# Optimization experiments

Hardware: AMD Instinct MI355X
Metric: run time of the kernel (lower is better)

Reference implementation:

```python
import jax, jax.numpy as jnp
import numpy as np

B, T, E, H, M2 = 8, 2048, 256, 2, 134
HD = E // H


def setup_inputs() -> dict:
    key = jax.random.key(0)
    ks = jax.random.split(key, 10)
    s = 0.02
    return {
        "X": jax.random.normal(ks[0], (B, T, E), dtype=jnp.float32),
        "Y": jax.random.uniform(ks[1], (B, M2), dtype=jnp.float32),
        "wpe": s * jax.random.normal(ks[2], (T, E), dtype=jnp.float32),
        "ln1_g": jnp.ones((E,), jnp.float32), "ln1_b": jnp.zeros((E,), jnp.float32),
        "attn_w": s * jax.random.normal(ks[3], (3 * E, E), dtype=jnp.float32),
        "attn_b": jnp.zeros((3 * E,), jnp.float32),
        "attnproj_w": s * jax.random.normal(ks[4], (E, E), dtype=jnp.float32),
        "attnproj_b": jnp.zeros((E,), jnp.float32),
        "ln2_g": jnp.ones((E,), jnp.float32), "ln2_b": jnp.zeros((E,), jnp.float32),
        "fc_w": s * jax.random.normal(ks[5], (2 * E, E), dtype=jnp.float32),
        "fc_b": jnp.zeros((2 * E,), jnp.float32),
        "mlpproj_w": s * jax.random.normal(ks[6], (E, 2 * E), dtype=jnp.float32),
        "mlpproj_b": jnp.zeros((E,), jnp.float32),
        "lnf_g": jnp.ones((E,), jnp.float32), "lnf_b": jnp.zeros((E,), jnp.float32),
        "head_w": s * jax.random.normal(ks[7], (M2, E), dtype=jnp.float32),
        "head_b": jnp.zeros((M2,), jnp.float32),
    }


def _ln(x, g, b, eps=1e-5):
    mu = x.mean(-1, keepdims=True)
    var = ((x - mu) ** 2).mean(-1, keepdims=True)
    return (x - mu) * jax.lax.rsqrt(var + eps) * g + b


def reference(X, Y, wpe, ln1_g, ln1_b, attn_w, attn_b, attnproj_w, attnproj_b,
              ln2_g, ln2_b, fc_w, fc_b, mlpproj_w, mlpproj_b, lnf_g, lnf_b,
              head_w, head_b):
    # positional ids = arange(T) -> wpe itself; cls ids = [0]*T/2 + [1]*T/2
    cls_ids = np.concatenate([np.zeros(T // 2, np.int32), np.ones(T // 2, np.int32)])
    x = X + wpe + wpe[cls_ids]                      # [B,T,E] (dropout = identity, eval)

    # single Block (n_layer=1), preceded by ReLU as in cross_mod loop
    x = jax.nn.relu(x)
    h = _ln(x, ln1_g, ln1_b)
    qkv = h @ attn_w.T + attn_b                     # [B,T,3E]
    q, k, v = jnp.split(qkv, 3, axis=-1)
    q, k, v = jax.nn.relu(q), jax.nn.relu(k), jax.nn.relu(v)
    split_heads = lambda t: t.reshape(B, T, H, HD).transpose(0, 2, 1, 3)
    q, k, v = split_heads(q), split_heads(k), split_heads(v)
    att = jnp.einsum('bhqd,bhkd->bhqk', q, k) * (1.0 / np.sqrt(HD))
    tril = jnp.tril(jnp.ones((T, T), dtype=bool))
    # masked_fill(-inf) then ReLU  ==  zero outside causal mask, ReLU inside
    att = jnp.where(tril, jax.nn.relu(att), 0.0)    # [B,H,T,T]
    y = jnp.einsum('bhqk,bhkd->bhqd', att, v)
    y = y.transpose(0, 2, 1, 3).reshape(B, T, E)
    x = x + (y @ attnproj_w.T + attnproj_b)

    h = _ln(x, ln2_g, ln2_b)
    x = x + (jax.nn.relu(h @ fc_w.T + fc_b) @ mlpproj_w.T + mlpproj_b)

    x = jax.nn.relu(x)
    x = _ln(x, lnf_g, lnf_b)
    x = jax.nn.relu(x)
    emb = x.mean(axis=1)                            # [B,E]
    logits = jax.nn.relu(emb @ head_w.T + head_b)   # [B,M2]

    loss1 = jnp.sqrt(jnp.mean((logits - Y) ** 2))
    e1, e2 = emb[:, : E // 2], emb[:, E // 2:]
    loss3 = jnp.sqrt(jnp.mean((e1 - e2) ** 2))
    loss = 50.0 * loss1 + loss3
    return (e1, e2, loss, loss1, loss3, logits)
```

## Files before the change

### kernel.cpp

```cpp
#include <hip/hip_runtime.h>
#include <hip/hip_bf16.h>

#define Bc 8
#define Tc 2048
#define Ec 256
#define Hc 2
#define HDc 128
#define Mrows (Bc*Tc)
#define M2c 134

using bfx8  = __attribute__((ext_vector_type(8))) __bf16;
using f32x4 = __attribute__((ext_vector_type(4))) float;

__device__ __forceinline__ void gll16(const __bf16* g, __bf16* lds) {
    __builtin_amdgcn_global_load_lds(
        (const __attribute__((address_space(1))) unsigned int*)g,
        (__attribute__((address_space(3))) unsigned int*)lds, 16, 0, 0);
}

__global__ __launch_bounds__(256) void embed_prep_k(const float* X, const float* wpe,
                                                    const float* g, const float* bb,
                                                    const float* attn_w, const float* apw,
                                                    const float* fcw, const float* mpw,
                                                    __bf16* wb, float* embsum,
                                                    __bf16* xres, __bf16* hb) {
    int m = blockIdx.x;
    int e = threadIdx.x;
    if (m < 2048) {
        int i = m * 256 + e;
        if (i < 196608)       wb[i] = (__bf16)attn_w[i];
        else if (i < 262144)  wb[i] = (__bf16)apw[i - 196608];
        else if (i < 393216)  wb[i] = (__bf16)fcw[i - 262144];
        else                  wb[i] = (__bf16)mpw[i - 393216];
        if (m < 8) embsum[m * 256 + e] = 0.f;
    }
    int t = m & (Tc - 1);
    float v = X[(size_t)m * Ec + e] + wpe[(size_t)t * Ec + e] + wpe[(size_t)(t >= 1024) * Ec + e];
    v = fmaxf(v, 0.f);
    xres[(size_t)m * Ec + e] = (__bf16)v;
    float s1 = v, s2 = v * v;
    #pragma unroll
    for (int o = 32; o; o >>= 1) { s1 += __shfl_xor(s1, o, 64); s2 += __shfl_xor(s2, o, 64); }
    __shared__ float a1[4], a2[4];
    int w = threadIdx.x >> 6;
    if ((threadIdx.x & 63) == 0) { a1[w] = s1; a2[w] = s2; }
    __syncthreads();
    float m1 = (a1[0] + a1[1] + a1[2] + a1[3]) * (1.f / 256.f);
    float m2 = (a2[0] + a2[1] + a2[2] + a2[3]) * (1.f / 256.f);
    float r = rsqrtf(m2 - m1 * m1 + 1e-5f);
    hb[(size_t)m * Ec + e] = (__bf16)((v - m1) * r * g[e] + bb[e]);
}

__global__ __launch_bounds__(256) void gemm_qkv(const __bf16* __restrict__ A,
                                                const __bf16* __restrict__ Bw,
                                                const float* __restrict__ bias,
                                                __bf16* __restrict__ Qb,
                                                __bf16* __restrict__ Kb,
                                                __bf16* __restrict__ Vb) {
    const int K = 256;
    __shared__ __bf16 As[128 * 64];
    __shared__ __bf16 Bs[128 * 64];
    const int tid = threadIdx.x, w = tid >> 6, l = tid & 63;
    const int m0 = blockIdx.y * 128, n0 = blockIdx.x * 128;
    const int wr = w >> 1, wc = w & 1;
    const int quad = l >> 4, col15 = l & 15;

    f32x4 acc[4][4];
    f32x4 zz = {0.f, 0.f, 0.f, 0.f};
    #pragma unroll
    for (int i = 0; i < 4; i++)
        #pragma unroll
        for (int j = 0; j < 4; j++) acc[i][j] = zz;

    const int lrow = l >> 3;
    const int pbs  = l & 7;

    for (int kb = 0; kb < K; kb += 64) {
        #pragma unroll
        for (int it = 0; it < 4; it++) {
            int chunk = w * 4 + it;
            int row = chunk * 8 + lrow;
            int lb = pbs ^ (row & 7);
            gll16(A  + (size_t)(m0 + row) * K + kb + lb * 8, As + chunk * 512);
            gll16(Bw + (size_t)(n0 + row) * K + kb + lb * 8, Bs + chunk * 512);
        }
        __syncthreads();
        #pragma unroll
        for (int ks = 0; ks < 2; ks++) {
            bfx8 af[4], bfr[4];
            #pragma unroll
            for (int rt = 0; rt < 4; rt++) {
                int row = wr * 64 + rt * 16 + col15;
                int pb = (ks * 4 + quad) ^ (row & 7);
                af[rt] = *(const bfx8*)(As + row * 64 + pb * 8);
            }
            #pragma unroll
            for (int ct = 0; ct < 4; ct++) {
                int row = wc * 64 + ct * 16 + col15;
                int pb = (ks * 4 + quad) ^ (row & 7);
                bfr[ct] = *(const bfx8*)(Bs + row * 64 + pb * 8);
            }
            #pragma unroll
            for (int rt = 0; rt < 4; rt++)
                #pragma unroll
                for (int ct = 0; ct < 4; ct++)
                    acc[rt][ct] = __builtin_amdgcn_mfma_f32_16x16x32_bf16(af[rt], bfr[ct], acc[rt][ct], 0, 0, 0);
        }
        __syncthreads();
    }

    #pragma unroll
    for (int rt = 0; rt < 4; rt++)
        #pragma unroll
        for (int ct = 0; ct < 4; ct++) {
            int mgb = m0 + wr * 64 + rt * 16 + quad * 4;
            int ng  = n0 + wc * 64 + ct * 16 + col15;
            float bsv = bias[ng];
            #pragma unroll
            for (int r = 0; r < 4; r++) {
                float val = fmaxf(acc[rt][ct][r] + bsv, 0.f);
                int mg = mgb + r;
                int sel = ng >> 8;
                int hh = (ng >> 7) & 1;
                int d = ng & 127;
                int bb = mg >> 11, tt = mg & (Tc - 1);
                size_t idx = ((size_t)((bb * 2 + hh) * Tc + tt)) * HDc + d;
                __bf16 bv = (__bf16)val;
                if (sel == 0) Qb[idx] = bv;
                else if (sel == 1) Kb[idx] = bv;
                else Vb[idx] = bv;
            }
        }
}

__global__ __launch_bounds__(256) void transpose_v(const unsigned short* Vb, unsigned short* Vt) {
    __shared__ unsigned short tile[64][66];
    int kt = blockIdx.x, dt = blockIdx.y, bh = blockIdx.z;
    int tid = threadIdx.x;
    int k0 = kt * 64, d0 = dt * 64;
    int rr = tid >> 4, cc = (tid & 15) * 4;
    #pragma unroll
    for (int p = 0; p < 4; p++) {
        int k = p * 16 + rr;
        const unsigned short* src = Vb + ((size_t)(bh * Tc + k0 + k)) * HDc + d0 + cc;
        ushort4 vv = *(const ushort4*)src;
        tile[k][cc] = vv.x; tile[k][cc + 1] = vv.y; tile[k][cc + 2] = vv.z; tile[k][cc + 3] = vv.w;
    }
    __syncthreads();
    #pragma unroll
    for (int p = 0; p < 4; p++) {
        int d = p * 16 + rr;
        unsigned short* dst = Vt + ((size_t)(bh * HDc + d0 + d)) * Tc + k0 + cc;
        ushort4 ov;
        ov.x = tile[cc][d]; ov.y = tile[cc + 1][d]; ov.z = tile[cc + 2][d]; ov.w = tile[cc + 3][d];
        *(ushort4*)dst = ov;
    }
}

__global__ __launch_bounds__(512, 4) void attn6_k(const __bf16* __restrict__ Qb,
                                                  const __bf16* __restrict__ Kb,
                                                  const __bf16* __restrict__ Vt,
                                                  __bf16* __restrict__ Y1,
                                                  __bf16* __restrict__ Y2,
                                                  __bf16* __restrict__ Y3,
                                                  __bf16* __restrict__ Y4) {
    __shared__ __bf16 Ks[2][64 * 128];
    __shared__ __bf16 Vs[2][64 * 128];
    __shared__ __bf16 Ss[128 * 64];
    int bid = blockIdx.x;
    int lane8 = bid & 7;
    int s = bid >> 3;
    int bh = ((s & 1) << 3) | lane8;
    int f = s >> 1;
    int qt, ch;
    if (f < 16)      { qt = 12 + (f >> 2);          ch = f & 3; }
    else if (f < 28) { int r = f - 16; int d3 = r / 3; qt = 8 + d3; ch = r - 3 * d3; }
    else if (f < 36) { qt = 4 + ((f - 28) >> 1);    ch = (f - 28) & 1; }
    else             { qt = f - 36;                 ch = 0; }
    int Q0 = qt * 128;
    int kts = ch * 8;
    int kte = min(kts + 8, 2 * qt + 2);

    int tid = threadIdx.x, w = tid >> 6, l = tid & 63;
    int quad = l >> 4, col15 = l & 15;
    const int qs = w >> 1, kh = w & 1;
    const int lrowK = l >> 4, pbsK = l & 15;
    const int lrowV = l >> 3, pbsV = l & 7;

    __bf16* Qs = &Ks[0][0];
    #pragma unroll
    for (int it = 0; it < 4; it++) {
        int chunk = w * 4 + it;
        int row = chunk * 4 + lrowK;
        int lb = pbsK ^ (row & 7);
        gll16(Qb + ((size_t)(bh * Tc + Q0 + row)) * HDc + lb * 8, Qs + chunk * 512);
    }
    __syncthreads();
    bfx8 qf[2][4];
    #pragma unroll
    for (int rt = 0; rt < 2; rt++)
        #pragma unroll
        for (int ks = 0; ks < 4; ks++) {
            int row = qs * 32 + rt * 16 + col15;
            int pb = (ks * 4 + quad) ^ (row & 7);
            qf[rt][ks] = *(const bfx8*)(Qs + row * 128 + pb * 8);
        }
    __syncthreads();

    f32x4 zz = {0.f, 0.f, 0.f, 0.f};
    f32x4 yacc[2][4];
    #pragma unroll
    for (int rt = 0; rt < 2; rt++)
        #pragma unroll
        for (int dt = 0; dt < 4; dt++) yacc[rt][dt] = zz;

    auto stageKV = [&](int buf, int kt) {
        #pragma unroll
        for (int it = 0; it < 2; it++) {
            int chunk = w * 2 + it;
            int rowK = chunk * 4 + lrowK;
            int lbK = pbsK ^ (rowK & 7);
            gll16(Kb + ((size_t)(bh * Tc + kt * 64 + rowK)) * HDc + lbK * 8, Ks[buf] + chunk * 512);
            int rowV = chunk * 8 + lrowV;
            int lbV = pbsV ^ (rowV & 7);
            gll16(Vt + ((size_t)(bh * HDc + rowV)) * Tc + kt * 64 + lbV * 8, Vs[buf] + chunk * 512);
        }
    };

    stageKV(0, kts);
    int cur = 0;
    for (int kt = kts; kt < kte; kt++) {
        __syncthreads();
        if (kt + 1 < kte) stageKV(cur ^ 1, kt + 1);

        f32x4 sacc[2][2];
        #pragma unroll
        for (int rt = 0; rt < 2; rt++)
            #pragma unroll
            for (int ct = 0; ct < 2; ct++) sacc[rt][ct] = zz;
        #pragma unroll
        for (int ks = 0; ks < 4; ks++) {
            #pragma unroll
            for (int ct = 0; ct < 2; ct++) {
                int row = kh * 32 + ct * 16 + col15;
                int pb = (ks * 4 + quad) ^ (row & 7);
                bfx8 kf = *(const bfx8*)(Ks[cur] + row * 128 + pb * 8);
                #pragma unroll
                for (int rt = 0; rt < 2; rt++)
                    sacc[rt][ct] = __builtin_amdgcn_mfma_f32_16x16x32_bf16(qf[rt][ks], kf, sacc[rt][ct], 0, 0, 0);
            }
        }

        #pragma unroll
        for (int ct = 0; ct < 2; ct++) {
            int kl = kh * 32 + ct * 16 + col15;
            int kg = kt * 64 + kl;
            int blk = kl >> 3, off = kl & 7;
            #pragma unroll
            for (int rt = 0; rt < 2; rt++)
                #pragma unroll
                for (int r = 0; r < 4; r++) {
                    int qlw = qs * 32 + rt * 16 + quad * 4 + r;
                    float val = (kg <= Q0 + qlw) ? fmaxf(sacc[rt][ct][r], 0.f) : 0.f;
                    int pb = blk ^ (qlw & 7);
                    Ss[qlw * 64 + pb * 8 + off] = (__bf16)val;
                }
        }

        asm volatile("s_waitcnt lgkmcnt(0)" ::: "memory");
        __builtin_amdgcn_s_barrier();
        __builtin_amdgcn_sched_barrier(0);

        #pragma unroll
        for (int ks = 0; ks < 2; ks++) {
            bfx8 sf[2];
            #pragma unroll
            for (int rt = 0; rt < 2; rt++) {
                int rowS = qs * 32 + rt * 16 + col15;
                int pbS = (ks * 4 + quad) ^ (rowS & 7);
                sf[rt] = *(const bfx8*)(Ss + rowS * 64 + pbS * 8);
            }
            #pragma unroll
            for (int dt = 0; dt < 4; dt++) {
                int rowV = kh * 64 + dt * 16 + col15;
                int pb = (ks * 4 + quad) ^ (rowV & 7);
                bfx8 vf = *(const bfx8*)(Vs[cur] + rowV * 64 + pb * 8);
                #pragma unroll
                for (int rt = 0; rt < 2; rt++)
                    yacc[rt][dt] = __builtin_amdgcn_mfma_f32_16x16x32_bf16(sf[rt], vf, yacc[rt][dt], 0, 0, 0);
            }
        }
        cur ^= 1;
    }

    __bf16* Yp = (ch == 0) ? Y1 : (ch == 1) ? Y2 : (ch == 2) ? Y3 : Y4;
    int b = bh >> 1, h = bh & 1;
    const float sc = 0.08838834764831845f;
    #pragma unroll
    for (int rt = 0; rt < 2; rt++)
        #pragma unroll
        for (int dt = 0; dt < 4; dt++) {
            int d = kh * 64 + dt * 16 + col15;
            #pragma unroll
            for (int r = 0; r < 4; r++) {
                int q = Q0 + qs * 32 + rt * 16 + quad * 4 + r;
                Yp[((size_t)(b * Tc + q)) * Ec + h * HDc + d] = (__bf16)(yacc[rt][dt][r] * sc);
            }
        }
}

__global__ __launch_bounds__(512, 1) void mega_k(const __bf16* __restrict__ Y1,
                                                 const __bf16* __restrict__ Y2,
                                                 const __bf16* __restrict__ Y3,
                                                 const __bf16* __restrict__ Y4,
                                                 const __bf16* __restrict__ wap,
                                                 const float* __restrict__ apb,
                                                 const __bf16* __restrict__ xres,
                                                 const float* __restrict__ ln2_g,
                                                 const float* __restrict__ ln2_b,
                                                 const __bf16* __restrict__ wfc,
                                                 const float* __restrict__ fcb,
                                                 const __bf16* __restrict__ wmp,
                                                 const float* __restrict__ mpb,
                                                 const float* __restrict__ lnf_g,
                                                 const float* __restrict__ lnf_b,
                                                 float* __restrict__ embsum) {
    __shared__ __bf16 h2s[4 * 4096];
    __shared__ __bf16 fc64[8 * 4096];
    __shared__ __bf16 Bs[256 * 64];
    __shared__ float ps1[64][8], ps2[64][8];
    __shared__ float mus[64], rss[64];
    const int tid = threadIdx.x, w = tid >> 6, l = tid & 63;
    const int m0 = blockIdx.x * 64;
    const int quad = l >> 4, col15 = l & 15;
    const int lrow = l >> 3, pbs = l & 7;
    const int n0 = w * 32;
    f32x4 zz = {0.f, 0.f, 0.f, 0.f};

    const int nsum = (((m0 & (Tc - 1)) >> 6) + 8) >> 3;
    __bf16* As = fc64;

    const int arow_s = tid >> 3;
    const int ablk   = tid & 7;

    auto loadY = [&](int kb) -> bfx8 {
        size_t off = (size_t)(m0 + arow_s) * 256 + kb + ablk * 8;
        bfx8 a1 = *(const bfx8*)(Y1 + off);
        float tmp[8];
        #pragma unroll
        for (int jj = 0; jj < 8; jj++) tmp[jj] = (float)a1[jj];
        if (nsum > 1) { bfx8 aj = *(const bfx8*)(Y2 + off);
            #pragma unroll
            for (int jj = 0; jj < 8; jj++) tmp[jj] += (float)aj[jj]; }
        if (nsum > 2) { bfx8 aj = *(const bfx8*)(Y3 + off);
            #pragma unroll
            for (int jj = 0; jj < 8; jj++) tmp[jj] += (float)aj[jj]; }
        if (nsum > 3) { bfx8 aj = *(const bfx8*)(Y4 + off);
            #pragma unroll
            for (int jj = 0; jj < 8; jj++) tmp[jj] += (float)aj[jj]; }
        #pragma unroll
        for (int jj = 0; jj < 8; jj++) a1[jj] = (__bf16)tmp[jj];
        return a1;
    };

    f32x4 acc[4][2];
    #pragma unroll
    for (int rt = 0; rt < 4; rt++)
        #pragma unroll
        for (int ct = 0; ct < 2; ct++) acc[rt][ct] = zz;

    bfx8 av = loadY(0);

    for (int kb = 0; kb < 256; kb += 64) {
        __syncthreads();
        { int pb = ablk ^ (arow_s & 7);
          *(bfx8*)(As + arow_s * 64 + pb * 8) = av; }
        #pragma unroll
        for (int it = 0; it < 4; it++) {
            int chunk = w * 4 + it;
            int row = chunk * 8 + lrow;
            int lb = pbs ^ (row & 7);
            gll16(wap + (size_t)row * 256 + kb + lb * 8, Bs + chunk * 512);
        }
        bfx8 avn;
        if (kb < 192) avn = loadY(kb + 64);
        __syncthreads();
        #pragma unroll
        for (int ks = 0; ks < 2; ks++) {
            bfx8 af[4];
            #pragma unroll
            for (int rt = 0; rt < 4; rt++) {
                int ar = rt * 16 + col15;
                int apbk = (ks * 4 + quad) ^ (ar & 7);
                af[rt] = *(const bfx8*)(As + ar * 64 + apbk * 8);
            }
            #pragma unroll
            for (int ct = 0; ct < 2; ct++) {
                int br = n0 + ct * 16 + col15;
                int bpb = (ks * 4 + quad) ^ (br & 7);
                bfx8 bf = *(const bfx8*)(Bs + br * 64 + bpb * 8);
                #pragma unroll
                for (int rt = 0; rt < 4; rt++)
                    acc[rt][ct] = __builtin_amdgcn_mfma_f32_16x16x32_bf16(af[rt], bf, acc[rt][ct], 0, 0, 0);
            }
        }
        if (kb < 192) av = avn;
    }

    float xv[4][2][4];
    #pragma unroll
    for (int ct = 0; ct < 2; ct++) {
        int ng = n0 + ct * 16 + col15;
        float bsv = apb[ng];
        #pragma unroll
        for (int rt = 0; rt < 4; rt++)
            #pragma unroll
            for (int r = 0; r < 4; r++) {
                int mg = m0 + rt * 16 + quad * 4 + r;
                xv[rt][ct][r] = acc[rt][ct][r] + bsv + (float)xres[(size_t)mg * 256 + ng];
            }
    }
    #pragma unroll
    for (int rt = 0; rt < 4; rt++)
        #pragma unroll
        for (int r = 0; r < 4; r++) {
            float a  = xv[rt][0][r] + xv[rt][1][r];
            float b2 = xv[rt][0][r] * xv[rt][0][r] + xv[rt][1][r] * xv[rt][1][r];
            #pragma unroll
            for (int o = 1; o < 16; o <<= 1) { a += __shfl_xor(a, o, 64); b2 += __shfl_xor(b2, o, 64); }
            if (col15 == 0) { int row = rt * 16 + quad * 4 + r; ps1[row][w] = a; ps2[row][w] = b2; }
        }
    __syncthreads();
    {
        int row = tid >> 3, widx = tid & 7;
        float a = ps1[row][widx], b2 = ps2[row][widx];
        #pragma unroll
        for (int o = 1; o < 8; o <<= 1) { a += __shfl_xor(a, o, 64); b2 += __shfl_xor(b2, o, 64); }
        if ((l & 7) == 0) {
            float mu = a * (1.f / 256.f);
            float var = b2 * (1.f / 256.f) - mu * mu;
            mus[row] = mu; rss[row] = rsqrtf(var + 1e-5f);
        }
    }
    __syncthreads();
    #pragma unroll
    for (int ct = 0; ct < 2; ct++) {
        int ng = n0 + ct * 16 + col15;
        float gv = ln2_g[ng], bv = ln2_b[ng];
        int panel = ng >> 6, c = ng & 63;
        #pragma unroll
        for (int rt = 0; rt < 4; rt++)
            #pragma unroll
            for (int r = 0; r < 4; r++) {
                int row = rt * 16 + quad * 4 + r;
                float h = (xv[rt][ct][r] - mus[row]) * rss[row] * gv + bv;
                h2s[panel * 4096 + row * 64 + ((c >> 3) ^ (row & 7)) * 8 + (c & 7)] = (__bf16)h;
            }
    }

    for (int half = 0; half < 2; half++) {
        f32x4 acc2[4][2];
        #pragma unroll
        for (int rt = 0; rt < 4; rt++)
            #pragma unroll
            for (int ct = 0; ct < 2; ct++) acc2[rt][ct] = zz;
        for (int kb = 0; kb < 256; kb += 64) {
            __syncthreads();
            #pragma unroll
            for (int it = 0; it < 4; it++) {
                int chunk = w * 4 + it;
                int row = chunk * 8 + lrow;
                int lb = pbs ^ (row & 7);
                gll16(wfc + (size_t)(half * 256 + row) * 256 + kb + lb * 8, Bs + chunk * 512);
            }
            __syncthreads();
            int panel = kb >> 6;
            #pragma unroll
            for (int ks = 0; ks < 2; ks++) {
                bfx8 af[4];
                #pragma unroll
                for (int rt = 0; rt < 4; rt++) {
                    int ar = rt * 16 + col15;
                    int apbk = (ks * 4 + quad) ^ (ar & 7);
                    af[rt] = *(const bfx8*)(h2s + panel * 4096 + ar * 64 + apbk * 8);
                }
                #pragma unroll
                for (int ct = 0; ct < 2; ct++) {
                    int br = n0 + ct * 16 + col15;
                    int bpb = (ks * 4 + quad) ^ (br & 7);
                    bfx8 bf = *(const bfx8*)(Bs + br * 64 + bpb * 8);
                    #pragma unroll
                    for (int rt = 0; rt < 4; rt++)
                        acc2[rt][ct] = __builtin_amdgcn_mfma_f32_16x16x32_bf16(af[rt], bf, acc2[rt][ct], 0, 0, 0);
                }
            }
        }
        #pragma unroll
        for (int ct = 0; ct < 2; ct++) {
            int col = half * 256 + n0 + ct * 16 + col15;
            float bsv = fcb[col];
            int panel = col >> 6, c = col & 63;
            #pragma unroll
            for (int rt = 0; rt < 4; rt++)
                #pragma unroll
                for (int r = 0; r < 4; r++) {
                    int row = rt * 16 + quad * 4 + r;
                    float val = fmaxf(acc2[rt][ct][r] + bsv, 0.f);
                    fc64[panel * 4096 + row * 64 + ((c >> 3) ^ (row & 7)) * 8 + (c & 7)] = (__bf16)val;
                }
        }
    }

    #pragma unroll
    for (int rt = 0; rt < 4; rt++)
        #pragma unroll
        for (int ct = 0; ct < 2; ct++) acc[rt][ct] = zz;
    for (int kb = 0; kb < 512; kb += 64) {
        __syncthreads();
        #pragma unroll
        for (int it = 0; it < 4; it++) {
            int chunk = w * 4 + it;
            int row = chunk * 8 + lrow;
            int lb = pbs ^ (row & 7);
            gll16(wmp + (size_t)row * 512 + kb + lb * 8, Bs + chunk * 512);
        }
        __syncthreads();
        int panel = kb >> 6;
        #pragma unroll
        for (int ks = 0; ks < 2; ks++) {
            bfx8 af[4];
            #pragma unroll
            for (int rt = 0; rt < 4; rt++) {
                int ar = rt * 16 + col15;
                int apbk = (ks * 4 + quad) ^ (ar & 7);
                af[rt] = *(const bfx8*)(fc64 + panel * 4096 + ar * 64 + apbk * 8);
            }
            #pragma unroll
            for (int ct = 0; ct < 2; ct++) {
                int br = n0 + ct * 16 + col15;
                int bpb = (ks * 4 + quad) ^ (br & 7);
                bfx8 bf = *(const bfx8*)(Bs + br * 64 + bpb * 8);
                #pragma unroll
                for (int rt = 0; rt < 4; rt++)
                    acc[rt][ct] = __builtin_amdgcn_mfma_f32_16x16x32_bf16(af[rt], bf, acc[rt][ct], 0, 0, 0);
            }
        }
    }

    #pragma unroll
    for (int ct = 0; ct < 2; ct++) {
        int ng = n0 + ct * 16 + col15;
        float bsv = mpb[ng];
        #pragma unroll
        for (int rt = 0; rt < 4; rt++)
            #pragma unroll
            for (int r = 0; r < 4; r++)
                xv[rt][ct][r] = fmaxf(acc[rt][ct][r] + bsv + xv[rt][ct][r], 0.f);
    }
    #pragma unroll
    for (int rt = 0; rt < 4; rt++)
        #pragma unroll
        for (int r = 0; r < 4; r++) {
            float a  = xv[rt][0][r] + xv[rt][1][r];
            float b2 = xv[rt][0][r] * xv[rt][0][r] + xv[rt][1][r] * xv[rt][1][r];
            #pragma unroll
            for (int o = 1; o < 16; o <<= 1) { a += __shfl_xor(a, o, 64); b2 += __shfl_xor(b2, o, 64); }
            if (col15 == 0) { int row = rt * 16 + quad * 4 + r; ps1[row][w] = a; ps2[row][w] = b2; }
        }
    __syncthreads();
    {
        int row = tid >> 3, widx = tid & 7;
        float a = ps1[row][widx], b2 = ps2[row][widx];
        #pragma unroll
        for (int o = 1; o < 8; o <<= 1) { a += __shfl_xor(a, o, 64); b2 += __shfl_xor(b2, o, 64); }
        if ((l & 7) == 0) {
            float mu = a * (1.f / 256.f);
            float var = b2 * (1.f / 256.f) - mu * mu;
            mus[row] = mu; rss[row] = rsqrtf(var + 1e-5f);
        }
    }
    __syncthreads();
    #pragma unroll
    for (int ct = 0; ct < 2; ct++) {
        int ng = n0 + ct * 16 + col15;
        float gv = lnf_g[ng], bv = lnf_b[ng];
        float csum = 0.f;
        #pragma unroll
        for (int rt = 0; rt < 4; rt++)
            #pragma unroll
            for (int r = 0; r < 4; r++) {
                int row = rt * 16 + quad * 4 + r;
                float h = (xv[rt][ct][r] - mus[row]) * rss[row] * gv + bv;
                csum += fmaxf(h, 0.f);
            }
        csum += __shfl_xor(csum, 16, 64);
        csum += __shfl_xor(csum, 32, 64);
        if (quad == 0) atomicAdd(&embsum[(m0 >> 11) * 256 + ng], csum);
    }
}

__global__ __launch_bounds__(256) void final_k(const float* embsum, const float* Yt,
                                               const float* head_w, const float* head_b,
                                               float* out) {
    __shared__ float semb[2048];
    __shared__ float slog[1072];
    int tid = threadIdx.x;
    for (int i = tid; i < 2048; i += 256) semb[i] = embsum[i] * (1.f / 2048.f);
    __syncthreads();
    float part1 = 0.f;
    for (int idx = tid; idx < 1072; idx += 256) {
        int b = idx / M2c, n = idx - b * M2c;
        float acc = head_b[n];
        const float* wn = head_w + (size_t)n * Ec;
        const float* e = semb + b * Ec;
        #pragma unroll 8
        for (int k = 0; k < Ec; k++) acc += e[k] * wn[k];
        acc = fmaxf(acc, 0.f);
        slog[idx] = acc;
        float d = acc - Yt[idx];
        part1 += d * d;
    }
    float part3 = 0.f;
    for (int idx = tid; idx < 1024; idx += 256) {
        int b = idx >> 7, i = idx & 127;
        float d = semb[b * Ec + i] - semb[b * Ec + 128 + i];
        part3 += d * d;
    }
    #pragma unroll
    for (int o = 32; o; o >>= 1) { part1 += __shfl_xor(part1, o, 64); part3 += __shfl_xor(part3, o, 64); }
    __shared__ float r1[4], r3[4];
    int w = tid >> 6;
    if ((tid & 63) == 0) { r1[w] = part1; r3[w] = part3; }
    __syncthreads();
    float l1 = sqrtf((r1[0] + r1[1] + r1[2] + r1[3]) / 1072.f);
    float l3 = sqrtf((r3[0] + r3[1] + r3[2] + r3[3]) / 1024.f);
    for (int idx = tid; idx < 1024; idx += 256) {
        int b = idx >> 7, i = idx & 127;
        out[idx]        = semb[b * Ec + i];
        out[1024 + idx] = semb[b * Ec + 128 + i];
    }
    if (tid == 0) {
        out[2048] = 50.f * l1 + l3;
        out[2049] = l1;
        out[2050] = l3;
    }
    for (int idx = tid; idx < 1072; idx += 256) out[2051 + idx] = slog[idx];
}

extern "C" void kernel_launch(void* const* d_in, const int* in_sizes, int n_in,
                              void* d_out, int out_size, void* d_ws, size_t ws_size,
                              hipStream_t stream) {
    const float* X        = (const float*)d_in[0];
    const float* Yt       = (const float*)d_in[1];
    const float* wpe      = (const float*)d_in[2];
    const float* ln1_g    = (const float*)d_in[3];
    const float* ln1_b    = (const float*)d_in[4];
    const float* attn_w   = (const float*)d_in[5];
    const float* attn_b   = (const float*)d_in[6];
    const float* apw      = (const float*)d_in[7];
    const float* apb      = (const float*)d_in[8];
    const float* ln2_g    = (const float*)d_in[9];
    const float* ln2_b    = (const float*)d_in[10];
    const float* fcw      = (const float*)d_in[11];
    const float* fcb      = (const float*)d_in[12];
    const float* mpw      = (const float*)d_in[13];
    const float* mpb      = (const float*)d_in[14];
    const float* lnf_g    = (const float*)d_in[15];
    const float* lnf_b    = (const float*)d_in[16];
    const float* head_w   = (const float*)d_in[17];
    const float* head_b   = (const float*)d_in[18];

    char* ws = (char*)d_ws;
    const size_t MB = 1048576;
    __bf16* xres   = (__bf16*)(ws + 0 * MB);
    __bf16* hb     = (__bf16*)(ws + 8 * MB);
    __bf16* Qb     = (__bf16*)(ws + 16 * MB);
    __bf16* Kb     = (__bf16*)(ws + 24 * MB);
    __bf16* Vb     = (__bf16*)(ws + 32 * MB);
    __bf16* Vt     = (__bf16*)(ws + 40 * MB);
    __bf16* Y1     = (__bf16*)(ws + 48 * MB);
    __bf16* Y2     = (__bf16*)(ws + 56 * MB);
    __bf16* wb     = (__bf16*)(ws + 64 * MB);
    float*  embsum = (float*)(ws + 65 * MB);

    __bf16* Y3 = hb;
    __bf16* Y4 = Vb;

    __bf16* wqkv = wb;
    __bf16* wap  = wb + 196608;
    __bf16* wfc  = wb + 262144;
    __bf16* wmp  = wb + 393216;

    embed_prep_k<<<Mrows, 256, 0, stream>>>(X, wpe, ln1_g, ln1_b,
                                            attn_w, apw, fcw, mpw, wb, embsum, xres, hb);
    gemm_qkv<<<dim3(6, 128), 256, 0, stream>>>(hb, wqkv, attn_b, Qb, Kb, Vb);
    transpose_v<<<dim3(32, 2, 16), 256, 0, stream>>>((const unsigned short*)Vb, (unsigned short*)Vt);
    attn6_k<<<640, 512, 0, stream>>>(Qb, Kb, Vt, Y1, Y2, Y3, Y4);
    mega_k<<<256, 512, 0, stream>>>(Y1, Y2, Y3, Y4, wap, apb, xres, ln2_g, ln2_b,
                                    wfc, fcb, wmp, mpb, lnf_g, lnf_b, embsum);
    final_k<<<1, 256, 0, stream>>>(embsum, Yt, head_w, head_b, (float*)d_out);
}
```

Before: 234.4 us.

## Fuse V transpose into QKV GEMM epilogue and vectorize embed/LN kernel

The QKV GEMM now writes V directly in transposed layout, staged through LDS, which removes the separate transpose_v kernel along with its extra global write and read of V. The embedding and LayerNorm kernel processes one row per wavefront using float4 loads and packed bf16 stores, so it no longer needs the block-wide shared-memory reduction and barrier. In exchange, GEMM shared memory grows to hold a 128x136 tile, which may reduce occupancy, and the V-tile blocks pay an extra barrier in their epilogue.

New measurement: 223.1 us. 4.8% less time.

```diff
diff --git a/kernel.cpp b/kernel.cpp
--- a/kernel.cpp
+++ b/kernel.cpp
@@ -10,6 +10,7 @@
 #define M2c 134
 
 using bfx8  = __attribute__((ext_vector_type(8))) __bf16;
+using bfx4  = __attribute__((ext_vector_type(4))) __bf16;
 using f32x4 = __attribute__((ext_vector_type(4))) float;
 
 __device__ __forceinline__ void gll16(const __bf16* g, __bf16* lds) {
@@ -24,31 +25,42 @@
                                                     const float* fcw, const float* mpw,
                                                     __bf16* wb, float* embsum,
                                                     __bf16* xres, __bf16* hb) {
-    int m = blockIdx.x;
-    int e = threadIdx.x;
-    if (m < 2048) {
-        int i = m * 256 + e;
+    int tid = threadIdx.x, w = tid >> 6, l = tid & 63;
+    int bidx = blockIdx.x;
+    if (bidx < 2048) {
+        int i = bidx * 256 + tid;
         if (i < 196608)       wb[i] = (__bf16)attn_w[i];
         else if (i < 262144)  wb[i] = (__bf16)apw[i - 196608];
         else if (i < 393216)  wb[i] = (__bf16)fcw[i - 262144];
         else                  wb[i] = (__bf16)mpw[i - 393216];
-        if (m < 8) embsum[m * 256 + e] = 0.f;
-    }
+        if (bidx < 8) embsum[bidx * 256 + tid] = 0.f;
+    }
+    int m = bidx * 4 + w;
     int t = m & (Tc - 1);
-    float v = X[(size_t)m * Ec + e] + wpe[(size_t)t * Ec + e] + wpe[(size_t)(t >= 1024) * Ec + e];
-    v = fmaxf(v, 0.f);
-    xres[(size_t)m * Ec + e] = (__bf16)v;
-    float s1 = v, s2 = v * v;
+    int e0 = l * 4;
+    float4 x  = *(const float4*)(X   + (size_t)m * Ec + e0);
+    float4 p1 = *(const float4*)(wpe + (size_t)t * Ec + e0);
+    float4 p2 = *(const float4*)(wpe + (size_t)(t >= 1024 ? Ec : 0) + e0);
+    float v0 = fmaxf(x.x + p1.x + p2.x, 0.f);
+    float v1 = fmaxf(x.y + p1.y + p2.y, 0.f);
+    float v2 = fmaxf(x.z + p1.z + p2.z, 0.f);
+    float v3 = fmaxf(x.w + p1.w + p2.w, 0.f);
+    bfx4 xq; xq[0] = (__bf16)v0; xq[1] = (__bf16)v1; xq[2] = (__bf16)v2; xq[3] = (__bf16)v3;
+    *(bfx4*)(xres + (size_t)m * Ec + e0) = xq;
+    float s1 = v0 + v1 + v2 + v3;
+    float s2 = v0 * v0 + v1 * v1 + v2 * v2 + v3 * v3;
     #pragma unroll
     for (int o = 32; o; o >>= 1) { s1 += __shfl_xor(s1, o, 64); s2 += __shfl_xor(s2, o, 64); }
-    __shared__ float a1[4], a2[4];
-    int w = threadIdx.x >> 6;
-    if ((threadIdx.x & 63) == 0) { a1[w] = s1; a2[w] = s2; }
-    __syncthreads();
-    float m1 = (a1[0] + a1[1] + a1[2] + a1[3]) * (1.f / 256.f);
-    float m2 = (a2[0] + a2[1] + a2[2] + a2[3]) * (1.f / 256.f);
+    float m1 = s1 * (1.f / 256.f), m2 = s2 * (1.f / 256.f);
     float r = rsqrtf(m2 - m1 * m1 + 1e-5f);
-    hb[(size_t)m * Ec + e] = (__bf16)((v - m1) * r * g[e] + bb[e]);
+    float4 gg = *(const float4*)(g + e0);
+    float4 bv = *(const float4*)(bb + e0);
+    bfx4 hq;
+    hq[0] = (__bf16)((v0 - m1) * r * gg.x + bv.x);
+    hq[1] = (__bf16)((v1 - m1) * r * gg.y + bv.y);
+    hq[2] = (__bf16)((v2 - m1) * r * gg.z + bv.z);
+    hq[3] = (__bf16)((v3 - m1) * r * gg.w + bv.w);
+    *(bfx4*)(hb + (size_t)m * Ec + e0) = hq;
 }
 
 __global__ __launch_bounds__(256) void gemm_qkv(const __bf16* __restrict__ A,
@@ -56,10 +68,11 @@
                                                 const float* __restrict__ bias,
                                                 __bf16* __restrict__ Qb,
                                                 __bf16* __restrict__ Kb,
-                                                __bf16* __restrict__ Vb) {
+                                                __bf16* __restrict__ Vt) {
     const int K = 256;
-    __shared__ __bf16 As[128 * 64];
-    __shared__ __bf16 Bs[128 * 64];
+    __shared__ __attribute__((aligned(16))) __bf16 smem[128 * 136];
+    __bf16* As = smem;
+    __bf16* Bs = smem + 128 * 64;
     const int tid = threadIdx.x, w = tid >> 6, l = tid & 63;
     const int m0 = blockIdx.y * 128, n0 = blockIdx.x * 128;
     const int wr = w >> 1, wc = w & 1;
@@ -109,51 +122,52 @@
         __syncthreads();
     }
 
-    #pragma unroll
-    for (int rt = 0; rt < 4; rt++)
-        #pragma unroll
-        for (int ct = 0; ct < 4; ct++) {
-            int mgb = m0 + wr * 64 + rt * 16 + quad * 4;
-            int ng  = n0 + wc * 64 + ct * 16 + col15;
-            float bsv = bias[ng];
-            #pragma unroll
-            for (int r = 0; r < 4; r++) {
-                float val = fmaxf(acc[rt][ct][r] + bsv, 0.f);
-                int mg = mgb + r;
-                int sel = ng >> 8;
-                int hh = (ng >> 7) & 1;
-                int d = ng & 127;
-                int bb = mg >> 11, tt = mg & (Tc - 1);
-                size_t idx = ((size_t)((bb * 2 + hh) * Tc + tt)) * HDc + d;
-                __bf16 bv = (__bf16)val;
-                if (sel == 0) Qb[idx] = bv;
-                else if (sel == 1) Kb[idx] = bv;
-                else Vb[idx] = bv;
-            }
-        }
-}
-
-__global__ __launch_bounds__(256) void transpose_v(const unsigned short* Vb, unsigned short* Vt) {
-    __shared__ unsigned short tile[64][66];
-    int kt = blockIdx.x, dt = blockIdx.y, bh = blockIdx.z;
-    int tid = threadIdx.x;
-    int k0 = kt * 64, d0 = dt * 64;
-    int rr = tid >> 4, cc = (tid & 15) * 4;
-    #pragma unroll
-    for (int p = 0; p < 4; p++) {
-        int k = p * 16 + rr;
-        const unsigned short* src = Vb + ((size_t)(bh * Tc + k0 + k)) * HDc + d0 + cc;
-        ushort4 vv = *(const ushort4*)src;
-        tile[k][cc] = vv.x; tile[k][cc + 1] = vv.y; tile[k][cc + 2] = vv.z; tile[k][cc + 3] = vv.w;
-    }
-    __syncthreads();
-    #pragma unroll
-    for (int p = 0; p < 4; p++) {
-        int d = p * 16 + rr;
-        unsigned short* dst = Vt + ((size_t)(bh * HDc + d0 + d)) * Tc + k0 + cc;
-        ushort4 ov;
-        ov.x = tile[cc][d]; ov.y = tile[cc + 1][d]; ov.z = tile[cc + 2][d]; ov.w = tile[cc + 3][d];
-        *(ushort4*)dst = ov;
+    if (n0 < 512) {
+        #pragma unroll
+        for (int rt = 0; rt < 4; rt++)
+            #pragma unroll
+            for (int ct = 0; ct < 4; ct++) {
+                int mgb = m0 + wr * 64 + rt * 16 + quad * 4;
+                int ng  = n0 + wc * 64 + ct * 16 + col15;
+                float bsv = bias[ng];
+                #pragma unroll
+                for (int r = 0; r < 4; r++) {
+                    float val = fmaxf(acc[rt][ct][r] + bsv, 0.f);
+                    int mg = mgb + r;
+                    int sel = ng >> 8;
+                    int hh = (ng >> 7) & 1;
+                    int d = ng & 127;
+                    int bb2 = mg >> 11, tt = mg & (Tc - 1);
+                    size_t idx = ((size_t)((bb2 * 2 + hh) * Tc + tt)) * HDc + d;
+                    __bf16 bv = (__bf16)val;
+                    if (sel == 0) Qb[idx] = bv;
+                    else Kb[idx] = bv;
+                }
+            }
+    } else {
+        int hh = (n0 >> 7) & 1;
+        int bh = (m0 >> 11) * 2 + hh;
+        #pragma unroll
+        for (int rt = 0; rt < 4; rt++)
+            #pragma unroll
+            for (int ct = 0; ct < 4; ct++) {
+                int d  = wc * 64 + ct * 16 + col15;
+                float bsv = bias[n0 + wc * 64 + ct * 16 + col15];
+                #pragma unroll
+                for (int r = 0; r < 4; r++) {
+                    int tt = wr * 64 + rt * 16 + quad * 4 + r;
+                    float val = fmaxf(acc[rt][ct][r] + bsv, 0.f);
+                    smem[d * 136 + tt] = (__bf16)val;
+                }
+            }
+        __syncthreads();
+        #pragma unroll
+        for (int it = 0; it < 8; it++) {
+            int d  = w * 32 + it * 4 + (l >> 4);
+            int t0 = (l & 15) * 8;
+            bfx8 vv = *(const bfx8*)(smem + d * 136 + t0);
+            *(bfx8*)(Vt + ((size_t)(bh * HDc + d)) * Tc + m0 + t0) = vv;
+        }
     }
 }
 
@@ -691,10 +705,9 @@
     __bf16* wfc  = wb + 262144;
     __bf16* wmp  = wb + 393216;
 
-    embed_prep_k<<<Mrows, 256, 0, stream>>>(X, wpe, ln1_g, ln1_b,
-                                            attn_w, apw, fcw, mpw, wb, embsum, xres, hb);
-    gemm_qkv<<<dim3(6, 128), 256, 0, stream>>>(hb, wqkv, attn_b, Qb, Kb, Vb);
-    transpose_v<<<dim3(32, 2, 16), 256, 0, stream>>>((const unsigned short*)Vb, (unsigned short*)Vt);
+    embed_prep_k<<<4096, 256, 0, stream>>>(X, wpe, ln1_g, ln1_b,
+                                           attn_w, apw, fcw, mpw, wb, embsum, xres, hb);
+    gemm_qkv<<<dim3(6, 128), 256, 0, stream>>>(hb, wqkv, attn_b, Qb, Kb, Vt);
     attn6_k<<<640, 512, 0, stream>>>(Qb, Kb, Vt, Y1, Y2, Y3, Y4);
     mega_k<<<256, 512, 0, stream>>>(Y1, Y2, Y3, Y4, wap, apb, xres, ln2_g, ln2_b,
                                     wfc, fcb, wmp, mpb, lnf_g, lnf_b, embsum);
```
